# Kernel tuning notes

Hardware: AMD Instinct MI355X
Metric: run time of the kernel (lower is better)

## Reference

```python
import jax, jax.numpy as jnp
import numpy as np

B, V, C, H, W = 4, 4, 20, 240, 320
M, N = 500000, 2000000   # unique voxels, full points
P, D, K = 100000, 64, 1024  # points per batch, proj dim, num_matches
TAU = 0.07
NEG = -1.0e6


def setup_inputs() -> dict:
    key = jax.random.key(0)
    ks = jax.random.split(key, 12)
    cam_3d_F = jax.random.normal(ks[0], (M, C), jnp.float32)
    cam_2d = jax.random.normal(ks[1], (B * V, C, H, W), jnp.float32)
    feat_proj_3d = jax.random.normal(ks[2], (B, P, D), jnp.float32)
    feat_detach_2d = jax.random.normal(ks[3], (B, P, D), jnp.float32)
    feat_proj_2d = jax.random.normal(ks[4], (B, P, D), jnp.float32)
    feat_detach_3d = jax.random.normal(ks[5], (B, P, D), jnp.float32)
    labels_cls_3d = (jax.random.uniform(ks[6], (B, C)) < 0.7).astype(jnp.float32).at[:, 0].set(1.0)
    labels_cls_2d = (jax.random.uniform(ks[7], (B, C)) < 0.7).astype(jnp.float32).at[:, 0].set(1.0)
    inverse_map = jax.random.randint(ks[8], (N,), 0, M)
    batch_idx = jnp.sort(jax.random.randint(ks[9], (N,), 0, B))
    # sample-without-replacement indices (np.random.choice replace=False analogue)
    match_idx_3d = jax.vmap(lambda k: jax.random.permutation(k, P)[:K])(jax.random.split(ks[10], B))
    match_idx_2d = jax.vmap(lambda k: jax.random.permutation(k, P)[:K])(jax.random.split(ks[11], B))
    return {
        "cam_3d_F": cam_3d_F, "cam_2d": cam_2d,
        "feat_proj_3d": feat_proj_3d, "feat_detach_2d": feat_detach_2d,
        "feat_proj_2d": feat_proj_2d, "feat_detach_3d": feat_detach_3d,
        "labels_cls_3d": labels_cls_3d, "labels_cls_2d": labels_cls_2d,
        "inverse_map": inverse_map, "batch_idx": batch_idx,
        "match_idx_3d": match_idx_3d, "match_idx_2d": match_idx_2d,
    }


def _soft_margin(x, y):
    # F.multilabel_soft_margin_loss: mean over classes then batch == overall mean
    return -jnp.mean(y * jax.nn.log_sigmoid(x) + (1.0 - y) * jax.nn.log_sigmoid(-x))


def _cmg_loss(fea_k, fea_q, idx):
    # fea_*: [B,P,D], idx: [B,K] -> InfoNCE with identity targets, summed over batches
    k = jnp.take_along_axis(fea_k, idx[:, :, None], axis=1)  # [B,K,D]
    q = jnp.take_along_axis(fea_q, idx[:, :, None], axis=1)  # [B,K,D]
    def one(kb, qb):
        logits = jnp.einsum('kd,md->km', kb, qb) / TAU  # [K,K]
        return -jnp.mean(jnp.diagonal(jax.nn.log_softmax(logits, axis=1)))
    return jnp.sum(jax.vmap(one)(k, q))


def reference(cam_3d_F, cam_2d, feat_proj_3d, feat_detach_2d, feat_proj_2d,
              feat_detach_3d, labels_cls_3d, labels_cls_2d,
              inverse_map, batch_idx, match_idx_3d, match_idx_2d):
    # ---- multi_class_loss_3d: gather + per-batch segment mean ----
    cam_full = cam_3d_F[inverse_map]                                   # [N,C]
    seg_sum = jax.ops.segment_sum(cam_full, batch_idx, num_segments=B)  # [B,C]
    cnt = jax.ops.segment_sum(jnp.ones((cam_full.shape[0],), cam_full.dtype),
                              batch_idx, num_segments=B)                # [B]
    cls_feat = seg_sum / cnt[:, None]
    loss_cam_3d = _soft_margin(cls_feat, labels_cls_3d)
    lab_full = labels_cls_3d[batch_idx]                                # [N,C]
    result_3d = jax.nn.softmax(cam_full + (1.0 - lab_full) * NEG, axis=1)
    # ---- multi_class_loss_2d ----
    cam2 = cam_2d.reshape(B, V, C, H, W).transpose(0, 2, 3, 4, 1)      # [B,C,H,W,V]
    predict_2d = cam2.mean(axis=(2, 3, 4))                             # mean over V then HxW
    loss_cam_2d = _soft_margin(predict_2d, labels_cls_2d)
    lab2 = labels_cls_2d[:, :, None, None, None]                       # [B,C,1,1,1]
    result_2d = jax.nn.softmax(cam2 + (1.0 - lab2) * NEG, axis=1)
    # ---- CMG contrastive losses (q side detached in the original) ----
    loss_cmg_3d = _cmg_loss(feat_proj_3d, jax.lax.stop_gradient(feat_detach_2d), match_idx_3d)
    loss_cmg_2d = _cmg_loss(feat_proj_2d, jax.lax.stop_gradient(feat_detach_3d), match_idx_2d)
    # warm weights and loss weights all 1.0 (post-warmup)
    loss = loss_cam_3d + loss_cam_2d + loss_cmg_3d + loss_cmg_2d
    return (loss, result_3d, result_2d)
```

## Files before the change

### kernel.cpp

```cpp
#include <hip/hip_runtime.h>

#define FLT_NEG_MAX -3.402823466e38f
#define NEGC -1000000.0f
#define INV_TAU (1.0f/0.07f)

static const long long NN = 2000000LL;

#define WS_KBUF 256
#define WS_PM   (WS_KBUF + 524288)
#define WS_PS   (WS_PM + 131072)
#define WS_DIAG (WS_PS + 131072)

__device__ __forceinline__ float wave_sum64(float v) {
  v += __shfl_xor(v, 1, 64);
  v += __shfl_xor(v, 2, 64);
  v += __shfl_xor(v, 4, 64);
  v += __shfl_xor(v, 8, 64);
  v += __shfl_xor(v, 16, 64);
  v += __shfl_xor(v, 32, 64);
  return v;
}
__device__ __forceinline__ float wave_max64(float v) {
  v = fmaxf(v, __shfl_xor(v, 1, 64));
  v = fmaxf(v, __shfl_xor(v, 2, 64));
  v = fmaxf(v, __shfl_xor(v, 4, 64));
  v = fmaxf(v, __shfl_xor(v, 8, 64));
  v = fmaxf(v, __shfl_xor(v, 16, 64));
  v = fmaxf(v, __shfl_xor(v, 32, 64));
  return v;
}
__device__ __forceinline__ float logsig(float x) {
  float z = -x;
  return -(fmaxf(z, 0.0f) + log1pf(__expf(-fabsf(z))));
}

__global__ __launch_bounds__(256) void kA(const float* __restrict__ cam3d,
                                          const float* __restrict__ lab3_g,
                                          const int* __restrict__ inv_map,
                                          const int* __restrict__ bidx,
                                          float* __restrict__ out_r3,
                                          float* __restrict__ acc) {
  __shared__ float lab3[80];
  __shared__ float bins[84];
  __shared__ float stage[4][64 * 21];
  const int tid = threadIdx.x;
  if (tid < 80) lab3[tid] = lab3_g[tid];
  if (tid < 84) bins[tid] = 0.0f;
  __syncthreads();
  const int wid = tid >> 6, lane = tid & 63;
  const long long stride = (long long)gridDim.x * 256LL;
  for (long long base = (long long)blockIdx.x * 256LL; base < NN; base += stride) {
    long long n = base + tid;
    bool active = (n < NN);
    float x[20];
    int b = 0;
    if (active) {
      int iv = inv_map[n];
      b = bidx[n];
      const float4* rp = reinterpret_cast<const float4*>(cam3d + (long long)iv * 20LL);
      #pragma unroll
      for (int q = 0; q < 5; ++q) {
        float4 t4 = rp[q];
        x[4*q+0] = t4.x; x[4*q+1] = t4.y; x[4*q+2] = t4.z; x[4*q+3] = t4.w;
      }
    } else {
      #pragma unroll
      for (int c = 0; c < 20; ++c) x[c] = 0.0f;
    }
    int b0 = __shfl(b, 0, 64);
    bool uni = __all(active) && __all(b == b0);
    if (uni) {
      #pragma unroll
      for (int c = 0; c < 20; ++c) {
        float v = wave_sum64(x[c]);
        if (lane == 0) atomicAdd(&bins[b0 * 20 + c], v);
      }
      if (lane == 0) atomicAdd(&bins[80 + b0], 64.0f);
    } else if (active) {
      #pragma unroll
      for (int c = 0; c < 20; ++c) atomicAdd(&bins[b * 20 + c], x[c]);
      atomicAdd(&bins[80 + b], 1.0f);
    }
    if (active) {
      float mx = FLT_NEG_MAX;
      #pragma unroll
      for (int c = 0; c < 20; ++c) {
        x[c] += (1.0f - lab3[b * 20 + c]) * NEGC;
        mx = fmaxf(mx, x[c]);
      }
      float s = 0.0f;
      #pragma unroll
      for (int c = 0; c < 20; ++c) { x[c] = __expf(x[c] - mx); s += x[c]; }
      float is = 1.0f / s;
      #pragma unroll
      for (int c = 0; c < 20; ++c) x[c] *= is;
    }
    __syncthreads();
    #pragma unroll
    for (int c = 0; c < 20; ++c) stage[wid][lane * 21 + c] = x[c];
    __syncthreads();
    long long nw = base + (long long)wid * 64LL;
    long long rem = NN - nw;
    int valid = rem >= 64 ? 64 : (rem > 0 ? (int)rem : 0);
    if (valid > 0) {
      int lim = valid * 20;
      #pragma unroll
      for (int j = 0; j < 20; ++j) {
        int idx = lane + 64 * j;
        if (idx < lim) {
          int rl = idx / 20;
          int cc = idx - rl * 20;
          __builtin_nontemporal_store(stage[wid][rl * 21 + cc],
                                      &out_r3[nw * 20LL + idx]);
        }
      }
    }
  }
  __syncthreads();
  if (tid < 84) atomicAdd(&acc[tid], bins[tid]);
}

__global__ __launch_bounds__(256) void kB(const float* __restrict__ cam2d,
                                          const float* __restrict__ lab2_g,
                                          float* __restrict__ out_r2,
                                          float* __restrict__ acc) {
  const int bid = blockIdx.x;
  const int b = bid / 1200;
  const int rem = bid - b * 1200;
  const int h = rem / 5;
  const int wt = rem - h * 5;
  const int t = threadIdx.x;
  const int wl = t >> 2, v = t & 3;
  const int w = wt * 64 + wl;
  const int lane = t & 63;
  __shared__ float bins2[20];
  if (t < 20) bins2[t] = 0.0f;
  __syncthreads();
  const float* inb = cam2d + ((long long)(b * 4 + v) * 20LL) * 76800LL + (long long)h * 320 + w;
  float x[20];
  #pragma unroll
  for (int c = 0; c < 20; ++c) x[c] = inb[(long long)c * 76800LL];
  #pragma unroll
  for (int c = 0; c < 20; ++c) {
    float s = wave_sum64(x[c]);
    if (lane == 0) atomicAdd(&bins2[c], s);
  }
  float mx = FLT_NEG_MAX;
  #pragma unroll
  for (int c = 0; c < 20; ++c) {
    x[c] += (1.0f - lab2_g[b * 20 + c]) * NEGC;
    mx = fmaxf(mx, x[c]);
  }
  float s = 0.0f;
  #pragma unroll
  for (int c = 0; c < 20; ++c) { x[c] = __expf(x[c] - mx); s += x[c]; }
  float is = 1.0f / s;
  #pragma unroll
  for (int c = 0; c < 20; ++c)
    __builtin_nontemporal_store(x[c] * is,
        &out_r2[(((long long)(b * 20 + c) * 240 + h) * 320 + w) * 4 + v]);
  __syncthreads();
  if (t < 20) atomicAdd(&acc[84 + b * 20 + t], bins2[t]);
}

__global__ __launch_bounds__(256) void kC(const float* __restrict__ fp3,
                                          const float* __restrict__ fp2,
                                          const int* __restrict__ mi3,
                                          const int* __restrict__ mi2,
                                          float* __restrict__ kbuf) {
  int g = blockIdx.x * 256 + threadIdx.x;
  int row = g >> 4;
  int d4 = g & 15;
  int pair = row >> 10;
  int l = pair >> 2, b = pair & 3;
  int i = row & 1023;
  int idx = l ? mi2[b * 1024 + i] : mi3[b * 1024 + i];
  const float* src = l ? fp2 : fp3;
  const float4* s4 = reinterpret_cast<const float4*>(src + ((long long)b * 100000 + idx) * 64LL);
  reinterpret_cast<float4*>(kbuf)[(long long)row * 16 + d4] = s4[d4];
}

__global__ __launch_bounds__(256) void kD(const float* __restrict__ kbuf,
                                          const float* __restrict__ fd2,
                                          const float* __restrict__ fd3,
                                          const int* __restrict__ mi3,
                                          const int* __restrict__ mi2,
                                          float* __restrict__ pm,
                                          float* __restrict__ ps,
                                          float* __restrict__ diag) {
  const int wglob = blockIdx.x * 4 + (threadIdx.x >> 6);
  const int lane = threadIdx.x & 63;
  const int pair = wglob >> 9;
  const int cb = (wglob >> 5) & 15;
  const int rb = wglob & 31;
  const int l = pair >> 2, b = pair & 3;
  const int colg = cb * 64 + lane;
  const int qi = l ? mi2[b * 1024 + colg] : mi3[b * 1024 + colg];
  const float* fq = l ? fd3 : fd2;
  const float4* q4 = reinterpret_cast<const float4*>(fq + ((long long)b * 100000 + qi) * 64LL);
  float4 q[16];
  #pragma unroll
  for (int d = 0; d < 16; ++d) q[d] = q4[d];
  const float* kbase = kbuf + ((long long)pair * 1024 + rb * 32) * 64LL;
  float m_keep = 0.0f, s_keep = 0.0f;
  for (int r = 0; r < 32; ++r) {
    const float4* kr = reinterpret_cast<const float4*>(kbase + r * 64);
    float a0 = 0, a1 = 0, a2 = 0, a3 = 0;
    #pragma unroll
    for (int d = 0; d < 16; ++d) {
      float4 kv = kr[d];
      a0 = fmaf(kv.x, q[d].x, a0);
      a1 = fmaf(kv.y, q[d].y, a1);
      a2 = fmaf(kv.z, q[d].z, a2);
      a3 = fmaf(kv.w, q[d].w, a3);
    }
    float vlog = (a0 + a1 + a2 + a3) * INV_TAU;
    int rowg = rb * 32 + r;
    if (colg == rowg) diag[pair * 1024 + rowg] = vlog;
    float mx = wave_max64(vlog);
    float se = wave_sum64(__expf(vlog - mx));
    if (lane == r) { m_keep = mx; s_keep = se; }
  }
  if (lane < 32) {
    int off = (pair * 16 + cb) * 1024 + rb * 32 + lane;
    pm[off] = m_keep;
    ps[off] = s_keep;
  }
}

__global__ __launch_bounds__(256) void kE(const float* __restrict__ pm,
                                          const float* __restrict__ ps,
                                          const float* __restrict__ diag,
                                          float* __restrict__ acc) {
  const int row = blockIdx.x * 256 + threadIdx.x;
  const int pair = row >> 10;
  const int rl = row & 1023;
  const int l = pair >> 2;
  float m = FLT_NEG_MAX, s = 0.0f;
  #pragma unroll
  for (int cb = 0; cb < 16; ++cb) {
    float mm = pm[(pair * 16 + cb) * 1024 + rl];
    float ss = ps[(pair * 16 + cb) * 1024 + rl];
    if (mm > m) { s = s * __expf(m - mm) + ss; m = mm; }
    else        { s += ss * __expf(mm - m); }
  }
  float r = diag[row] - (m + __logf(s));
  float t = wave_sum64(r);
  __shared__ float wsum[4];
  if ((threadIdx.x & 63) == 0) wsum[threadIdx.x >> 6] = t;
  __syncthreads();
  if (threadIdx.x == 0)
    atomicAdd(&acc[164 + l], wsum[0] + wsum[1] + wsum[2] + wsum[3]);
}

__global__ __launch_bounds__(256) void kF(const float* __restrict__ acc,
                                          const float* __restrict__ lab3,
                                          const float* __restrict__ lab2,
                                          float* __restrict__ out_loss) {
  const int t = threadIdx.x;
  float term = 0.0f;
  if (t < 80) {
    int b = t / 20;
    float x = acc[t] / acc[80 + b];
    float y = lab3[t];
    term = y * logsig(x) + (1.0f - y) * logsig(-x);
  } else if (t < 160) {
    int i = t - 80;
    float x = acc[84 + i] * (1.0f / 307200.0f);
    float y = lab2[i];
    term = y * logsig(x) + (1.0f - y) * logsig(-x);
  }
  float tsum = wave_sum64(term);
  __shared__ float wsum[4];
  if ((t & 63) == 0) wsum[t >> 6] = tsum;
  __syncthreads();
  if (t == 0) {
    float total = wsum[0] + wsum[1] + wsum[2] + wsum[3];
    float margin = -total / 80.0f;
    float cmg = -(acc[164] + acc[165]) / 1024.0f;
    out_loss[0] = margin + cmg;
  }
}

extern "C" void kernel_launch(void* const* d_in, const int* in_sizes, int n_in,
                              void* d_out, int out_size, void* d_ws, size_t ws_size,
                              hipStream_t stream) {
  (void)in_sizes; (void)n_in; (void)out_size; (void)ws_size;
  const float* cam3d = (const float*)d_in[0];
  const float* cam2d = (const float*)d_in[1];
  const float* fp3   = (const float*)d_in[2];
  const float* fd2   = (const float*)d_in[3];
  const float* fp2   = (const float*)d_in[4];
  const float* fd3   = (const float*)d_in[5];
  const float* lab3  = (const float*)d_in[6];
  const float* lab2  = (const float*)d_in[7];
  const int* invm    = (const int*)d_in[8];
  const int* bidx    = (const int*)d_in[9];
  const int* mi3     = (const int*)d_in[10];
  const int* mi2     = (const int*)d_in[11];

  float* out      = (float*)d_out;
  float* out_loss = out;
  float* out_r3   = out + 1;
  float* out_r2   = out + 1 + 40000000LL;

  float* acc  = (float*)d_ws;
  float* kbuf = acc + WS_KBUF;
  float* pm   = acc + WS_PM;
  float* psb  = acc + WS_PS;
  float* diag = acc + WS_DIAG;

  hipMemsetAsync(d_ws, 0, 1024, stream);

  kA<<<2048, 256, 0, stream>>>(cam3d, lab3, invm, bidx, out_r3, acc);
  kB<<<4800, 256, 0, stream>>>(cam2d, lab2, out_r2, acc);
  kC<<<512, 256, 0, stream>>>(fp3, fp2, mi3, mi2, kbuf);
  kD<<<1024, 256, 0, stream>>>(kbuf, fd2, fd3, mi3, mi2, pm, psb, diag);
  kE<<<32, 256, 0, stream>>>(pm, psb, diag, acc);
  kF<<<1, 256, 0, stream>>>(acc, lab3, lab2, out_loss);
}
```

Measured before the change: 716.8 us.

## Defer kA batch reductions in registers and coalesce kB loads via LDS transpose

In kA, per-lane running sums for the current batch are kept in registers and reduced across the wave only when the batch index changes, instead of a 20-channel wave reduction plus LDS atomics every iteration. In kB, each wave now reads one view's contiguous w range, so loads coalesce fully; results are transposed through a shared-memory buffer so the interleaved-view output stays contiguous. kA's grid is also shrunk. The changes add register pressure in kA and extra LDS traffic plus a barrier in kB.

```diff
diff --git a/kernel.cpp b/kernel.cpp
--- a/kernel.cpp
+++ b/kernel.cpp
@@ -48,6 +48,13 @@
   if (tid < 84) bins[tid] = 0.0f;
   __syncthreads();
   const int wid = tid >> 6, lane = tid & 63;
+
+  float racc[20];
+  #pragma unroll
+  for (int c = 0; c < 20; ++c) racc[c] = 0.0f;
+  float rcnt = 0.0f;
+  int rb_cur = -1;
+
   const long long stride = (long long)gridDim.x * 256LL;
   for (long long base = (long long)blockIdx.x * 256LL; base < NN; base += stride) {
     long long n = base + tid;
@@ -70,12 +77,22 @@
     int b0 = __shfl(b, 0, 64);
     bool uni = __all(active) && __all(b == b0);
     if (uni) {
-      #pragma unroll
-      for (int c = 0; c < 20; ++c) {
-        float v = wave_sum64(x[c]);
-        if (lane == 0) atomicAdd(&bins[b0 * 20 + c], v);
+      if (b0 != rb_cur) {
+        if (rb_cur >= 0) {
+          #pragma unroll
+          for (int c = 0; c < 20; ++c) {
+            float v = wave_sum64(racc[c]);
+            if (lane == 0) atomicAdd(&bins[rb_cur * 20 + c], v);
+            racc[c] = 0.0f;
+          }
+          if (lane == 0) atomicAdd(&bins[80 + rb_cur], rcnt * 64.0f);
+          rcnt = 0.0f;
+        }
+        rb_cur = b0;
       }
-      if (lane == 0) atomicAdd(&bins[80 + b0], 64.0f);
+      #pragma unroll
+      for (int c = 0; c < 20; ++c) racc[c] += x[c];
+      rcnt += 1.0f;
     } else if (active) {
       #pragma unroll
       for (int c = 0; c < 20; ++c) atomicAdd(&bins[b * 20 + c], x[c]);
@@ -115,6 +132,14 @@
         }
       }
     }
+  }
+  if (rb_cur >= 0) {
+    #pragma unroll
+    for (int c = 0; c < 20; ++c) {
+      float v = wave_sum64(racc[c]);
+      if (lane == 0) atomicAdd(&bins[rb_cur * 20 + c], v);
+    }
+    if (lane == 0) atomicAdd(&bins[80 + rb_cur], rcnt * 64.0f);
   }
   __syncthreads();
   if (tid < 84) atomicAdd(&acc[tid], bins[tid]);
@@ -130,13 +155,15 @@
   const int h = rem / 5;
   const int wt = rem - h * 5;
   const int t = threadIdx.x;
-  const int wl = t >> 2, v = t & 3;
-  const int w = wt * 64 + wl;
+  const int wid = t >> 6;
   const int lane = t & 63;
+  const int w = wt * 64 + lane;
   __shared__ float bins2[20];
+  __shared__ float trans[20][320];
   if (t < 20) bins2[t] = 0.0f;
   __syncthreads();
-  const float* inb = cam2d + ((long long)(b * 4 + v) * 20LL) * 76800LL + (long long)h * 320 + w;
+  const float* inb = cam2d + ((long long)(b * 4 + wid) * 20LL) * 76800LL
+                   + (long long)h * 320 + w;
   float x[20];
   #pragma unroll
   for (int c = 0; c < 20; ++c) x[c] = inb[(long long)c * 76800LL];
@@ -156,10 +183,13 @@
   for (int c = 0; c < 20; ++c) { x[c] = __expf(x[c] - mx); s += x[c]; }
   float is = 1.0f / s;
   #pragma unroll
+  for (int c = 0; c < 20; ++c) trans[c][lane * 5 + wid] = x[c] * is;
+  __syncthreads();
+  const long long obase = (long long)b * 6144000LL + ((long long)h * 320 + wt * 64) * 4LL;
+  #pragma unroll
   for (int c = 0; c < 20; ++c)
-    __builtin_nontemporal_store(x[c] * is,
-        &out_r2[(((long long)(b * 20 + c) * 240 + h) * 320 + w) * 4 + v]);
-  __syncthreads();
+    __builtin_nontemporal_store(trans[c][(t >> 2) * 5 + (t & 3)],
+                                &out_r2[obase + (long long)c * 307200LL + t]);
   if (t < 20) atomicAdd(&acc[84 + b * 20 + t], bins2[t]);
 }
 
@@ -312,7 +342,7 @@
 
   hipMemsetAsync(d_ws, 0, 1024, stream);
 
-  kA<<<2048, 256, 0, stream>>>(cam3d, lab3, invm, bidx, out_r3, acc);
+  kA<<<1792, 256, 0, stream>>>(cam3d, lab3, invm, bidx, out_r3, acc);
   kB<<<4800, 256, 0, stream>>>(cam2d, lab2, out_r2, acc);
   kC<<<512, 256, 0, stream>>>(fp3, fp2, mi3, mi2, kbuf);
   kD<<<1024, 256, 0, stream>>>(kbuf, fd2, fd3, mi3, mi2, pm, psb, diag);
```

Result: no change. 716.7 us (-0.0%).
